# Kernel tuning notes

Hardware: AMD Instinct MI355X
Metric: run time of the kernel (lower is better)

## Reference

```python
import jax, jax.numpy as jnp
import numpy as np

B, S, D, H, DFF, L, R, V = 2, 1024, 1024, 16, 4096, 2, 3, 32000
HD = D // H


def layer_norm(x, g, b, eps=1e-5):
    mu = jnp.mean(x, axis=-1, keepdims=True)
    var = jnp.var(x, axis=-1, keepdims=True)
    return (x - mu) / jnp.sqrt(var + eps) * g + b


def recursion_block(x, mask, Wqkv, bqkv, Wo, bo, W1, b1, W2, b2, ln1_g, ln1_b, ln2_g, ln2_b):
    # shared pre-LN transformer stack of L layers, applied once per recursion step
    Bc, Sc, _ = x.shape
    scale = 1.0 / np.sqrt(HD).astype(np.float32)
    for l in range(L):
        h = layer_norm(x, ln1_g[l], ln1_b[l])
        qkv = h @ Wqkv[l] + bqkv[l]
        q, k, v = jnp.split(qkv, 3, axis=-1)
        q = q.reshape(Bc, Sc, H, HD).transpose(0, 2, 1, 3)
        k = k.reshape(Bc, Sc, H, HD).transpose(0, 2, 1, 3)
        v = v.reshape(Bc, Sc, H, HD).transpose(0, 2, 1, 3)
        scores = jnp.einsum('bhqd,bhkd->bhqk', q, k) * scale + mask
        attn = jax.nn.softmax(scores, axis=-1)
        o = jnp.einsum('bhqk,bhkd->bhqd', attn, v).transpose(0, 2, 1, 3).reshape(Bc, Sc, D)
        x = x + o @ Wo[l] + bo[l]
        h2 = layer_norm(x, ln2_g[l], ln2_b[l])
        x = x + jax.nn.gelu(h2 @ W1[l] + b1[l]) @ W2[l] + b2[l]
    return x


def setup_inputs() -> dict:
    key = jax.random.key(0)
    ks = jax.random.split(key, 12)
    n = lambda k, shape: (jax.random.normal(k, shape, jnp.float32) * 0.02)
    return {
        'input_ids': jax.random.randint(ks[0], (B, S), 0, V),
        'token_embed': n(ks[1], (V, D)),
        'pos_embed': n(ks[2], (S, D)),
        'Wqkv': n(ks[3], (L, D, 3 * D)), 'bqkv': jnp.zeros((L, 3 * D), jnp.float32),
        'Wo': n(ks[4], (L, D, D)), 'bo': jnp.zeros((L, D), jnp.float32),
        'W1': n(ks[5], (L, D, DFF)), 'b1': jnp.zeros((L, DFF), jnp.float32),
        'W2': n(ks[6], (L, DFF, D)), 'b2': jnp.zeros((L, D), jnp.float32),
        'ln1_g': jnp.ones((L, D), jnp.float32), 'ln1_b': jnp.zeros((L, D), jnp.float32),
        'ln2_g': jnp.ones((L, D), jnp.float32), 'ln2_b': jnp.zeros((L, D), jnp.float32),
        'final_g': jnp.ones((D,), jnp.float32), 'final_b': jnp.zeros((D,), jnp.float32),
        'Wr': n(ks[7], (D, R)), 'br': jnp.zeros((R,), jnp.float32),
    }


def reference(input_ids, token_embed, pos_embed, Wqkv, bqkv, Wo, bo, W1, b1, W2, b2,
              ln1_g, ln1_b, ln2_g, ln2_b, final_g, final_b, Wr, br):
    h = token_embed[input_ids] + pos_embed[None, :, :]            # [B,S,D]
    mask = jnp.where(jnp.tril(jnp.ones((S, S), bool)), 0.0, -jnp.inf)[None, None]  # [1,1,S,S]
    # token-choice router on detached hidden states
    rlogits = jax.lax.stop_gradient(h) @ Wr + br                  # [B,S,R]
    probs = jax.nn.softmax(rlogits, axis=-1)
    depth_map = jnp.argmax(rlogits, axis=-1) + 1                  # depths in 1..R
    importance = probs.mean(axis=(0, 1))
    router_loss = R * jnp.sum(importance ** 2)                    # load-balance aux loss
    res = h
    for step in range(R):
        step_mask = depth_map >= step + 1                         # [B,S] bool
        upd = recursion_block(res, mask, Wqkv, bqkv, Wo, bo, W1, b1, W2, b2,
                              ln1_g, ln1_b, ln2_g, ln2_b)
        res = jnp.where(step_mask[..., None], upd, res)
    hf = layer_norm(res, final_g, final_b)
    logits = hf @ token_embed.T                                   # tied lm_head
    return logits, depth_map, router_loss
```

## Files before the change

kernel.cpp:

```cpp
#include <hip/hip_runtime.h>
#include <hip/hip_bf16.h>

#define DD 1024
#define SS 1024
#define BB 2
#define HH 16
#define DFFN 4096
#define LLAYERS 2
#define RSTEPS 3
#define VV 32000
#define NTOK (BB*SS)

typedef __attribute__((ext_vector_type(8))) short s16x8;
typedef __attribute__((ext_vector_type(8))) __bf16 bf16x8;
typedef __attribute__((ext_vector_type(4))) float f32x4;

__device__ __forceinline__ unsigned short f2bf(float f) {
  unsigned int u = __float_as_uint(f);
  u += 0x7FFFu + ((u >> 16) & 1u);
  return (unsigned short)(u >> 16);
}

__device__ __forceinline__ f32x4 mfma16(s16x8 a, s16x8 b, f32x4 c) {
  return __builtin_amdgcn_mfma_f32_16x16x32_bf16(
      __builtin_bit_cast(bf16x8, a), __builtin_bit_cast(bf16x8, b), c, 0, 0, 0);
}

__device__ __forceinline__ void gload16(const unsigned short* g, unsigned short* l) {
  __builtin_amdgcn_global_load_lds(
      (const __attribute__((address_space(1))) unsigned int*)(const void*)g,
      (__attribute__((address_space(3))) unsigned int*)(void*)l, 16, 0, 0);
}

#define BAR()  asm volatile("s_barrier" ::: "memory")
#define LGK0() do { asm volatile("s_waitcnt lgkmcnt(0)" ::: "memory"); \
                    __builtin_amdgcn_sched_barrier(0); } while (0)
#define VM4()  asm volatile("s_waitcnt vmcnt(4)" ::: "memory")
#define VM0()  asm volatile("s_waitcnt vmcnt(0)" ::: "memory")

__global__ __launch_bounds__(256) void wtrans_all_kernel(
    const float* __restrict__ Wqkv, const float* __restrict__ Wo,
    const float* __restrict__ W1, const float* __restrict__ W2,
    unsigned short* __restrict__ WqkvT, unsigned short* __restrict__ WoT,
    unsigned short* __restrict__ W1T, unsigned short* __restrict__ W2T) {
  const int bid = blockIdx.x;
  const float* src; unsigned short* dst; int Kd, Nd, local;
  if (bid < 1536) {
    int l = bid >> 9 >= 1 ? (bid >= 768) : 0; l = (bid >= 768);
    local = bid - l * 768;
    src = Wqkv + (long)l * DD * 3 * DD; dst = WqkvT + (long)l * 3 * DD * DD;
    Kd = DD; Nd = 3 * DD;
  } else if (bid < 2048) {
    int l = (bid - 1536) >> 8; local = (bid - 1536) & 255;
    src = Wo + (long)l * DD * DD; dst = WoT + (long)l * DD * DD;
    Kd = DD; Nd = DD;
  } else if (bid < 4096) {
    int l = (bid - 2048) >> 10; local = (bid - 2048) & 1023;
    src = W1 + (long)l * DD * DFFN; dst = W1T + (long)l * DFFN * DD;
    Kd = DD; Nd = DFFN;
  } else {
    int l = (bid - 4096) >> 10; local = (bid - 4096) & 1023;
    src = W2 + (long)l * DFFN * DD; dst = W2T + (long)l * DD * DFFN;
    Kd = DFFN; Nd = DD;
  }
  const int tn = Nd >> 6;
  const int n0 = (local % tn) * 64, k0 = (local / tn) * 64;
  __shared__ unsigned short t[64][68];
  const int tid = threadIdx.x;
#pragma unroll
  for (int c = 0; c < 4; ++c) {
    int p = tid + c * 256;
    int kr = p >> 4, nc = (p & 15) * 4;
    float4 v = *(const float4*)(src + (long)(k0 + kr) * Nd + n0 + nc);
    t[nc + 0][kr] = f2bf(v.x);
    t[nc + 1][kr] = f2bf(v.y);
    t[nc + 2][kr] = f2bf(v.z);
    t[nc + 3][kr] = f2bf(v.w);
  }
  __syncthreads();
#pragma unroll
  for (int c = 0; c < 4; ++c) {
    int p = tid + c * 256;
    int nr = p >> 4, kc = (p & 15) * 4;
    ushort4 o;
    o.x = t[nr][kc]; o.y = t[nr][kc + 1]; o.z = t[nr][kc + 2]; o.w = t[nr][kc + 3];
    *(ushort4*)(dst + (long)(n0 + nr) * Kd + k0 + kc) = o;
  }
}

__global__ __launch_bounds__(256) void bconv_kernel(
    const float* __restrict__ src, unsigned short* __restrict__ dst) {
  long i = ((long)blockIdx.x * 256 + threadIdx.x) * 8;
  float4 v0 = *(const float4*)(src + i);
  float4 v1 = *(const float4*)(src + i + 4);
  ushort4 a, b;
  a.x = f2bf(v0.x); a.y = f2bf(v0.y); a.z = f2bf(v0.z); a.w = f2bf(v0.w);
  b.x = f2bf(v1.x); b.y = f2bf(v1.y); b.z = f2bf(v1.z); b.w = f2bf(v1.w);
  *(ushort4*)(dst + i) = a;
  *(ushort4*)(dst + i + 4) = b;
}

__global__ __launch_bounds__(256) void embed_router_kernel(
    const int* __restrict__ ids, const float* __restrict__ te,
    const float* __restrict__ pe, const float* __restrict__ Wr,
    const float* __restrict__ br, float* __restrict__ res,
    float* __restrict__ probs, float* __restrict__ depth_ws,
    float* __restrict__ out_depth) {
  int row = blockIdx.x;
  int s = row & (SS - 1);
  int id = ids[row];
  int t = threadIdx.x;
  int d = t * 4;
  float4 a = *(const float4*)(te + (long)id * DD + d);
  float4 p = *(const float4*)(pe + (long)s * DD + d);
  float4 o; o.x = a.x + p.x; o.y = a.y + p.y; o.z = a.z + p.z; o.w = a.w + p.w;
  *(float4*)(res + (long)row * DD + d) = o;
  float a0 = 0.f, a1 = 0.f, a2 = 0.f;
  float hv[4] = {o.x, o.y, o.z, o.w};
#pragma unroll
  for (int j = 0; j < 4; ++j) {
    int dd = d + j;
    a0 += hv[j] * Wr[dd * 3 + 0];
    a1 += hv[j] * Wr[dd * 3 + 1];
    a2 += hv[j] * Wr[dd * 3 + 2];
  }
  for (int off = 32; off; off >>= 1) {
    a0 += __shfl_down(a0, off);
    a1 += __shfl_down(a1, off);
    a2 += __shfl_down(a2, off);
  }
  __shared__ float red[4][3];
  int wave = t >> 6;
  if ((t & 63) == 0) { red[wave][0] = a0; red[wave][1] = a1; red[wave][2] = a2; }
  __syncthreads();
  if (t == 0) {
    a0 = red[0][0] + red[1][0] + red[2][0] + red[3][0] + br[0];
    a1 = red[0][1] + red[1][1] + red[2][1] + red[3][1] + br[1];
    a2 = red[0][2] + red[1][2] + red[2][2] + red[3][2] + br[2];
    float m = fmaxf(a0, fmaxf(a1, a2));
    float e0 = expf(a0 - m), e1 = expf(a1 - m), e2 = expf(a2 - m);
    float inv = 1.f / (e0 + e1 + e2);
    probs[row * 3 + 0] = e0 * inv;
    probs[row * 3 + 1] = e1 * inv;
    probs[row * 3 + 2] = e2 * inv;
    int am = 0; float bv = a0;
    if (a1 > bv) { bv = a1; am = 1; }
    if (a2 > bv) { bv = a2; am = 2; }
    float dm = (float)(am + 1);
    depth_ws[row] = dm;
    out_depth[row] = dm;
  }
}

__global__ __launch_bounds__(256) void router_finalize_kernel(
    const float* __restrict__ probs, float* __restrict__ out_loss) {
  __shared__ float red[256][3];
  int t = threadIdx.x;
  float s0 = 0.f, s1 = 0.f, s2 = 0.f;
  for (int r = t; r < NTOK; r += 256) {
    s0 += probs[r * 3 + 0]; s1 += probs[r * 3 + 1]; s2 += probs[r * 3 + 2];
  }
  red[t][0] = s0; red[t][1] = s1; red[t][2] = s2;
  __syncthreads();
  for (int off = 128; off; off >>= 1) {
    if (t < off) {
      red[t][0] += red[t + off][0];
      red[t][1] += red[t + off][1];
      red[t][2] += red[t + off][2];
    }
    __syncthreads();
  }
  if (t == 0) {
    float i0 = red[0][0] / NTOK, i1 = red[0][1] / NTOK, i2 = red[0][2] / NTOK;
    out_loss[0] = (float)RSTEPS * (i0 * i0 + i1 * i1 + i2 * i2);
  }
}

__global__ __launch_bounds__(256) void ln_kernel(
    const float* __restrict__ x, const float* __restrict__ g,
    const float* __restrict__ b, unsigned short* __restrict__ y) {
  int row = blockIdx.x;
  int t = threadIdx.x;
  float4 v = *(const float4*)(x + (long)row * DD + t * 4);
  float s = v.x + v.y + v.z + v.w;
  float q = v.x * v.x + v.y * v.y + v.z * v.z + v.w * v.w;
  for (int off = 32; off; off >>= 1) {
    s += __shfl_down(s, off);
    q += __shfl_down(q, off);
  }
  __shared__ float rs[4], rq[4];
  int wave = t >> 6;
  if ((t & 63) == 0) { rs[wave] = s; rq[wave] = q; }
  __syncthreads();
  float S_ = rs[0] + rs[1] + rs[2] + rs[3];
  float Q_ = rq[0] + rq[1] + rq[2] + rq[3];
  float mu = S_ * (1.f / DD);
  float var = Q_ * (1.f / DD) - mu * mu;
  float rstd = rsqrtf(var + 1e-5f);
  int d = t * 4;
  float4 gg = *(const float4*)(g + d);
  float4 bb = *(const float4*)(b + d);
  ushort4 ov;
  ov.x = f2bf((v.x - mu) * rstd * gg.x + bb.x);
  ov.y = f2bf((v.y - mu) * rstd * gg.y + bb.y);
  ov.z = f2bf((v.z - mu) * rstd * gg.z + bb.z);
  ov.w = f2bf((v.w - mu) * rstd * gg.w + bb.w);
  *(ushort4*)(y + (long)row * DD + d) = ov;
}

__device__ __forceinline__ void stageA8(unsigned short* S, int buf, int qm,
    const unsigned short* A, int lda, long m0, int kt, int tid) {
  unsigned short* dst = S + buf * 32768 + qm * 8192;
#pragma unroll
  for (int c = 0; c < 2; ++c) {
    int idx = tid + c * 512;
    int L = (idx << 4) ^ (((idx >> 5) & 1) << 5);
    int band = L >> 13, row = (L >> 7) & 63, kel = (L & 127) >> 1;
    gload16(A + (m0 + band * 128 + qm * 64 + row) * (long)lda + kt * 64 + kel,
            dst + idx * 8);
  }
}

__device__ __forceinline__ void stageB8(unsigned short* S, int buf, int qn,
    const unsigned short* Bt, int ldb, long n0, int kt, int tid) {
  unsigned short* dst = S + buf * 32768 + 16384 + qn * 8192;
#pragma unroll
  for (int c = 0; c < 2; ++c) {
    int idx = tid + c * 512;
    int L = (idx << 4) ^ (((idx >> 5) & 1) << 5);
    int band = L >> 12, row = (L >> 7) & 31, kel = (L & 127) >> 1;
    gload16(Bt + (n0 + band * 64 + qn * 32 + row) * (long)ldb + kt * 64 + kel,
            dst + idx * 8);
  }
}

__device__ __forceinline__ void read_af8(const unsigned short* S, int base,
    int wm, int l16, int g, s16x8 af[2][4]) {
  const int swz = ((l16 >> 2) & 1) << 5;
#pragma unroll
  for (int kk = 0; kk < 2; ++kk)
#pragma unroll
    for (int mf = 0; mf < 4; ++mf) {
      int L = (wm * 8192 + (mf * 16 + l16) * 128 + (kk * 32 + g * 8) * 2) ^ swz;
      af[kk][mf] = *(const s16x8*)(S + base + (L >> 1));
    }
}

__device__ __forceinline__ void read_bf8(const unsigned short* S, int base,
    int wn, int l16, int g, s16x8 bf[2][2]) {
  const int swz = ((l16 >> 2) & 1) << 5;
#pragma unroll
  for (int kk = 0; kk < 2; ++kk)
#pragma unroll
    for (int nf = 0; nf < 2; ++nf) {
      int L = (wn * 4096 + (nf * 16 + l16) * 128 + (kk * 32 + g * 8) * 2) ^ swz;
      bf[kk][nf] = *(const s16x8*)(S + base + (L >> 1));
    }
}

template<int QM, int QN>
__device__ __forceinline__ void do_mfma8(f32x4 acc[8][4],
    const s16x8 af[2][4], const s16x8 bf[2][2]) {
  __builtin_amdgcn_s_setprio(1);
#pragma unroll
  for (int kk = 0; kk < 2; ++kk)
#pragma unroll
    for (int mf = 0; mf < 4; ++mf)
#pragma unroll
      for (int nf = 0; nf < 2; ++nf)
        acc[QM * 4 + mf][QN * 2 + nf] =
            mfma16(af[kk][mf], bf[kk][nf], acc[QM * 4 + mf][QN * 2 + nf]);
  __builtin_amdgcn_s_setprio(0);
}

template<int CBF16, int BIAS, int GELU_ACT>
__global__ __launch_bounds__(512, 1) void gemm256_kernel(
    const unsigned short* __restrict__ A, int lda,
    const unsigned short* __restrict__ Bt, int ldb,
    void* __restrict__ Cv, int ldc,
    const float* __restrict__ bias, int K, int Mblocks) {
  __shared__ unsigned short S[65536];
  const int tid = threadIdx.x;
  const int lane = tid & 63, wave = tid >> 6;
  const int g = lane >> 4, l16 = lane & 15;
  const int wm = wave >> 2, wn = wave & 3;
  const int nwg = gridDim.x * gridDim.y;
  const int orig = blockIdx.x + blockIdx.y * gridDim.x;
  const int q = nwg >> 3, r = nwg & 7;
  const int xcd = orig & 7, loc = orig >> 3;
  const int wgid = (xcd < r ? xcd * (q + 1) : r * (q + 1) + (xcd - r) * q) + loc;
  const long m0 = (long)(wgid % Mblocks) * 256;
  const long n0 = (long)(wgid / Mblocks) * 256;

  f32x4 acc[8][4] = {};
  s16x8 af[2][4], bf[2][2];
  const int NI = K >> 7;

  stageA8(S, 0, 0, A, lda, m0, 0, tid);
  stageA8(S, 0, 1, A, lda, m0, 0, tid);
  stageB8(S, 0, 0, Bt, ldb, n0, 0, tid);
  stageB8(S, 0, 1, Bt, ldb, n0, 0, tid);
  stageA8(S, 1, 0, A, lda, m0, 1, tid);
  stageB8(S, 1, 1, Bt, ldb, n0, 1, tid);
  VM4(); BAR();

  for (int i = 0; i < NI; ++i) {
    const int kt1 = 2 * i + 1, kt2 = 2 * i + 2, kt3 = 2 * i + 3;
    const bool more = (i + 1 < NI);
    read_af8(S, 0, wm, l16, g, af);
    read_bf8(S, 16384, wn, l16, g, bf);
    stageA8(S, 1, 1, A, lda, m0, kt1, tid);
    BAR(); LGK0();
    do_mfma8<0, 0>(acc, af, bf);
    BAR();
    read_bf8(S, 16384 + 8192, wn, l16, g, bf);
    stageB8(S, 1, 0, Bt, ldb, n0, kt1, tid);
    BAR(); LGK0();
    do_mfma8<0, 1>(acc, af, bf);
    BAR();
    read_af8(S, 8192, wm, l16, g, af);
    if (more) stageA8(S, 0, 0, A, lda, m0, kt2, tid);
    BAR(); LGK0();
    do_mfma8<1, 1>(acc, af, bf);
    BAR();
    read_bf8(S, 16384, wn, l16, g, bf);
    if (more) stageB8(S, 0, 1, Bt, ldb, n0, kt2, tid);
    BAR(); LGK0();
    do_mfma8<1, 0>(acc, af, bf);
    if (more) { VM4(); } else { VM0(); }
    BAR();
    read_af8(S, 32768, wm, l16, g, af);
    read_bf8(S, 32768 + 16384, wn, l16, g, bf);
    if (more) stageA8(S, 0, 1, A, lda, m0, kt2, tid);
    BAR(); LGK0();
    do_mfma8<0, 0>(acc, af, bf);
    BAR();
    read_bf8(S, 32768 + 16384 + 8192, wn, l16, g, bf);
    if (more) stageB8(S, 0, 0, Bt, ldb, n0, kt2, tid);
    BAR(); LGK0();
    do_mfma8<0, 1>(acc, af, bf);
    BAR();
    read_af8(S, 32768 + 8192, wm, l16, g, af);
    if (more) stageA8(S, 1, 0, A, lda, m0, kt3, tid);
    BAR(); LGK0();
    do_mfma8<1, 1>(acc, af, bf);
    BAR();
    read_bf8(S, 32768 + 16384, wn, l16, g, bf);
    if (more) stageB8(S, 1, 1, Bt, ldb, n0, kt3, tid);
    BAR(); LGK0();
    do_mfma8<1, 0>(acc, af, bf);
    VM4(); BAR();
  }

#pragma unroll
  for (int mf = 0; mf < 8; ++mf) {
#pragma unroll
    for (int nf = 0; nf < 4; ++nf) {
      long row0 = m0 + wm * 128 + mf * 16 + g * 4;
      long col = n0 + wn * 64 + nf * 16 + l16;
      float bv = BIAS ? bias[col] : 0.f;
#pragma unroll
      for (int rr = 0; rr < 4; ++rr) {
        float v = acc[mf][nf][rr] + bv;
        if (GELU_ACT) {
          float x3 = v * v * v;
          v = 0.5f * v * (1.f + tanhf(0.7978845608028654f * (v + 0.044715f * x3)));
        }
        if (CBF16) ((unsigned short*)Cv)[(row0 + rr) * (long)ldc + col] = f2bf(v);
        else       ((float*)Cv)[(row0 + rr) * (long)ldc + col] = v;
      }
    }
  }
}

template<int BN, int CBF16, int BIAS, int RESID, int GELU_ACT, int SELW>
__global__ __launch_bounds__(256) void gemm128_kernel(
    const unsigned short* __restrict__ A, int lda,
    const unsigned short* __restrict__ Bt, int ldb,
    void* __restrict__ Cv, int ldc,
    const float* __restrict__ bias,
    const float* __restrict__ resid, int ldr,
    const float* __restrict__ depth_ws, float stepf,
    int K) {
  constexpr int BM = 128;
  constexpr int WN = BN / 2;
  constexpr int MR = 4;
  constexpr int NR = WN / 16;
  __shared__ unsigned short As[BM * 64];
  __shared__ unsigned short Bs[BN * 64];
  const int tid = threadIdx.x;
  const int lane = tid & 63, wave = tid >> 6;
  const int g = lane >> 4, l16 = lane & 15;
  const int wr = wave >> 1, wc = wave & 1;
  int lin = blockIdx.x + blockIdx.y * gridDim.x;
  int per = (gridDim.x * gridDim.y) >> 3;
  int v = (lin & 7) * per + (lin >> 3);
  const long m0 = (long)(v % gridDim.y) * BM;
  const long n0 = (long)(v / gridDim.y) * BN;
  f32x4 acc[MR][NR] = {};
  for (int k0 = 0; k0 < K; k0 += 64) {
    __syncthreads();
#pragma unroll
    for (int c = 0; c < BM / 32; ++c) {
      int p = tid + c * 256;
      int r = p >> 3, kq = (p & 7) * 8;
      gload16(A + (m0 + r) * (long)lda + k0 + kq, &As[p * 8]);
    }
#pragma unroll
    for (int c = 0; c < BN / 32; ++c) {
      int p = tid + c * 256;
      int r = p >> 3, kq = (p & 7) * 8;
      gload16(Bt + (n0 + r) * (long)ldb + k0 + kq, &Bs[p * 8]);
    }
    __syncthreads();
#pragma unroll
    for (int kk = 0; kk < 2; ++kk) {
      s16x8 af[MR], bf[NR];
#pragma unroll
      for (int m = 0; m < MR; ++m)
        af[m] = *(const s16x8*)&As[(wr * 64 + m * 16 + l16) * 64 + kk * 32 + g * 8];
#pragma unroll
      for (int n = 0; n < NR; ++n)
        bf[n] = *(const s16x8*)&Bs[(wc * WN + n * 16 + l16) * 64 + kk * 32 + g * 8];
#pragma unroll
      for (int m = 0; m < MR; ++m)
#pragma unroll
        for (int n = 0; n < NR; ++n)
          acc[m][n] = mfma16(af[m], bf[n], acc[m][n]);
    }
  }
#pragma unroll
  for (int m = 0; m < MR; ++m) {
#pragma unroll
    for (int n = 0; n < NR; ++n) {
      long row_base = m0 + wr * 64 + m * 16 + g * 4;
      long col = n0 + wc * WN + n * 16 + l16;
      float bv = BIAS ? bias[col] : 0.f;
#pragma unroll
      for (int r = 0; r < 4; ++r) {
        long row = row_base + r;
        float vv = acc[m][n][r] + bv;
        if (RESID) vv += resid[row * (long)ldr + col];
        if (GELU_ACT) {
          float x3 = vv * vv * vv;
          vv = 0.5f * vv * (1.f + tanhf(0.7978845608028654f * (vv + 0.044715f * x3)));
        }
        if (SELW) {
          if (depth_ws[row] >= stepf)
            ((float*)Cv)[row * (long)ldc + col] = vv;
        } else if (CBF16) {
          ((unsigned short*)Cv)[row * (long)ldc + col] = f2bf(vv);
        } else {
          ((float*)Cv)[row * (long)ldc + col] = vv;
        }
      }
    }
  }
}

__global__ __launch_bounds__(256) void vtrans_kernel(
    const unsigned short* __restrict__ qkv, unsigned short* __restrict__ vt) {
  __shared__ unsigned short t[64][72];
  const int s0 = blockIdx.x * 64;
  const int bh = blockIdx.y;
  const int b = bh >> 4, h = bh & 15;
  const int tid = threadIdx.x;
  const long rowbase = (long)b * SS;
#pragma unroll
  for (int c = 0; c < 2; ++c) {
    int p = tid + c * 256;
    int sr = p >> 3, d8 = (p & 7) * 8;
    s16x8 v = *(const s16x8*)(qkv + (rowbase + s0 + sr) * 3072 + 2048 + h * 64 + d8);
#pragma unroll
    for (int j = 0; j < 8; ++j) t[d8 + j][sr] = v[j];
  }
  __syncthreads();
#pragma unroll
  for (int c = 0; c < 2; ++c) {
    int p = tid + c * 256;
    int d = p >> 3, s8 = (p & 7) * 8;
    *(s16x8*)(vt + ((long)bh * 64 + d) * SS + s0 + s8) = *(const s16x8*)&t[d][s8];
  }
}

__global__ __launch_bounds__(256) void attn_kernel(
    const unsigned short* __restrict__ qkv,
    const unsigned short* __restrict__ vt,
    unsigned short* __restrict__ o) {
  __shared__ unsigned short Ks[2][64 * 64];
  __shared__ unsigned short Vs[2][64 * 64];
  __shared__ unsigned short Pl[4][16][72];
  const int qb = blockIdx.x;
  const int bh = blockIdx.y;
  const int b = bh >> 4, h = bh & 15;
  const int tid = threadIdx.x, wave = tid >> 6, lane = tid & 63;
  const int g = lane >> 4, l16 = lane & 15;
  const float NEG_INF = -__builtin_inff();
  const int q0 = qb * 64;
  const int qrw = q0 + wave * 16;
  const long rowbase = (long)b * SS;
  const unsigned short* kbase = qkv + rowbase * 3072 + 1024 + h * 64;
  const unsigned short* vbase = vt + (long)bh * 64 * SS;

  const unsigned short* qptr = qkv + (rowbase + qrw + l16) * 3072 + h * 64;
  s16x8 qf0 = *(const s16x8*)(qptr + g * 8);
  s16x8 qf1 = *(const s16x8*)(qptr + 32 + g * 8);

  f32x4 oacc[4] = {};
  float mrun = NEG_INF, lrun = 0.f;

  const int ntile = q0 / 64 + 1;

#pragma unroll
  for (int c = 0; c < 2; ++c) {
    int idx = tid + c * 256;
    int r = idx >> 3;
    int bo = (idx & 7) * 16;
    int sw = (bo ^ ((r & 7) << 4)) >> 1;
    gload16(kbase + (long)r * 3072 + sw, &Ks[0][idx * 8]);
    gload16(vbase + (long)r * SS + 0 + sw, &Vs[0][idx * 8]);
  }
  asm volatile("s_waitcnt vmcnt(0)" ::: "memory");
  __syncthreads();

  for (int t = 0; t < ntile; ++t) {
    const int cur = t & 1;
    const int kv0 = t * 64;
    const unsigned short* ks_cur = &Ks[cur][0];
    const unsigned short* vs_cur = &Vs[cur][0];
    if (t + 1 < ntile) {
      const int kvn = kv0 + 64;
#pragma unroll
      for (int c = 0; c < 2; ++c) {
        int idx = tid + c * 256;
        int r = idx >> 3;
        int bo = (idx & 7) * 16;
        int sw = (bo ^ ((r & 7) << 4)) >> 1;
        gload16(kbase + (long)(kvn + r) * 3072 + sw, &Ks[cur ^ 1][idx * 8]);
        gload16(vbase + (long)r * SS + kvn + sw, &Vs[cur ^ 1][idx * 8]);
      }
    }
    f32x4 accs[4] = {};
#pragma unroll
    for (int ks = 0; ks < 2; ++ks) {
#pragma unroll
      for (int kvb = 0; kvb < 4; ++kvb) {
        int row = kvb * 16 + l16;
        int bo = ((ks * 64 + g * 16) ^ ((l16 & 7) << 4)) >> 1;
        s16x8 kf = *(const s16x8*)&ks_cur[row * 64 + bo];
        accs[kvb] = mfma16(kf, ks ? qf1 : qf0, accs[kvb]);
      }
    }
    const bool needmask = (kv0 + 63 > qrw);
    const int qabs = qrw + l16;
    float sv[4][4];
    float mloc = NEG_INF;
#pragma unroll
    for (int kvb = 0; kvb < 4; ++kvb) {
#pragma unroll
      for (int r = 0; r < 4; ++r) {
        float vv = accs[kvb][r] * 0.125f;
        if (needmask) {
          int kva = kv0 + kvb * 16 + g * 4 + r;
          if (kva > qabs) vv = NEG_INF;
        }
        sv[kvb][r] = vv;
        mloc = fmaxf(mloc, vv);
      }
    }
    mloc = fmaxf(mloc, __shfl_xor(mloc, 16));
    mloc = fmaxf(mloc, __shfl_xor(mloc, 32));
    float mnew = fmaxf(mrun, mloc);
    float alpha = __expf(mrun - mnew);
    float lsum = 0.f;
#pragma unroll
    for (int kvb = 0; kvb < 4; ++kvb) {
      float p0 = __expf(sv[kvb][0] - mnew);
      float p1 = __expf(sv[kvb][1] - mnew);
      float p2 = __expf(sv[kvb][2] - mnew);
      float p3 = __expf(sv[kvb][3] - mnew);
      lsum += (p0 + p1) + (p2 + p3);
      unsigned int w0 = (unsigned)f2bf(p0) | ((unsigned)f2bf(p1) << 16);
      unsigned int w1 = (unsigned)f2bf(p2) | ((unsigned)f2bf(p3) << 16);
      uint2 pw; pw.x = w0; pw.y = w1;
      *(uint2*)&Pl[wave][l16][kvb * 16 + g * 4] = pw;
    }
    lsum += __shfl_xor(lsum, 16);
    lsum += __shfl_xor(lsum, 32);
    lrun = lrun * alpha + lsum;
    mrun = mnew;
    float mult[4];
#pragma unroll
    for (int r = 0; r < 4; ++r) mult[r] = __shfl(alpha, g * 4 + r);
#pragma unroll
    for (int nd = 0; nd < 4; ++nd)
#pragma unroll
      for (int r = 0; r < 4; ++r) oacc[nd][r] *= mult[r];
#pragma unroll
    for (int kh = 0; kh < 2; ++kh) {
      s16x8 pa = *(const s16x8*)&Pl[wave][l16][kh * 32 + g * 8];
#pragma unroll
      for (int nd = 0; nd < 4; ++nd) {
        int row = nd * 16 + l16;
        int bo = ((kh * 64 + g * 16) ^ ((l16 & 7) << 4)) >> 1;
        s16x8 vf = *(const s16x8*)&vs_cur[row * 64 + bo];
        oacc[nd] = mfma16(pa, vf, oacc[nd]);
      }
    }
    asm volatile("s_waitcnt vmcnt(0)" ::: "memory");
    __syncthreads();
  }
  unsigned short* ob = o + (rowbase + qrw) * 1024 + h * 64;
#pragma unroll
  for (int r = 0; r < 4; ++r) {
    float lr = __shfl(lrun, g * 4 + r);
    float inv = 1.f / lr;
#pragma unroll
    for (int nd = 0; nd < 4; ++nd)
      ob[(long)(g * 4 + r) * 1024 + nd * 16 + l16] = f2bf(oacc[nd][r] * inv);
  }
}

extern "C" void kernel_launch(void* const* d_in, const int* in_sizes, int n_in,
                              void* d_out, int out_size, void* d_ws, size_t ws_size,
                              hipStream_t stream) {
  (void)in_sizes; (void)n_in; (void)out_size; (void)ws_size;
  const int*   ids  = (const int*)d_in[0];
  const float* te   = (const float*)d_in[1];
  const float* pe   = (const float*)d_in[2];
  const float* Wqkv = (const float*)d_in[3];
  const float* bqkv = (const float*)d_in[4];
  const float* Wo   = (const float*)d_in[5];
  const float* bo   = (const float*)d_in[6];
  const float* W1   = (const float*)d_in[7];
  const float* b1   = (const float*)d_in[8];
  const float* W2   = (const float*)d_in[9];
  const float* b2   = (const float*)d_in[10];
  const float* ln1g = (const float*)d_in[11];
  const float* ln1b = (const float*)d_in[12];
  const float* ln2g = (const float*)d_in[13];
  const float* ln2b = (const float*)d_in[14];
  const float* fing = (const float*)d_in[15];
  const float* finb = (const float*)d_in[16];
  const float* Wr   = (const float*)d_in[17];
  const float* br   = (const float*)d_in[18];

  float* logits    = (float*)d_out;
  float* out_depth = logits + (long)NTOK * VV;
  float* out_loss  = out_depth + NTOK;

  char* w = (char*)d_ws;
  float* res            = (float*)w;          w += (long)NTOK * DD * 4;
  float* x              = (float*)w;          w += (long)NTOK * DD * 4;
  unsigned short* hbuf  = (unsigned short*)w; w += (long)NTOK * DD * 2;
  unsigned short* qkvb  = (unsigned short*)w; w += (long)NTOK * 3 * DD * 2;
  unsigned short* obuf  = (unsigned short*)w; w += (long)NTOK * DD * 2;
  unsigned short* ffn1  = (unsigned short*)w; w += (long)NTOK * DFFN * 2;
  unsigned short* vtb   = (unsigned short*)w; w += (long)BB * HH * 64 * SS * 2;
  float* probs          = (float*)w;          w += (long)NTOK * 3 * 4;
  float* depth_ws       = (float*)w;          w += (long)NTOK * 4;
  unsigned short* WqkvT = (unsigned short*)w; w += (long)LLAYERS * 3 * DD * DD * 2;
  unsigned short* WoT   = (unsigned short*)w; w += (long)LLAYERS * DD * DD * 2;
  unsigned short* W1T   = (unsigned short*)w; w += (long)LLAYERS * DFFN * DD * 2;
  unsigned short* W2T   = (unsigned short*)w; w += (long)LLAYERS * DD * DFFN * 2;
  unsigned short* teb   = (unsigned short*)w; w += (long)VV * DD * 2;

  wtrans_all_kernel<<<6144, 256, 0, stream>>>(Wqkv, Wo, W1, W2,
                                              WqkvT, WoT, W1T, W2T);
  bconv_kernel<<<(long)VV * DD / 2048, 256, 0, stream>>>(te, teb);

  embed_router_kernel<<<NTOK, 256, 0, stream>>>(ids, te, pe, Wr, br,
                                                res, probs, depth_ws, out_depth);
  router_finalize_kernel<<<1, 256, 0, stream>>>(probs, out_loss);

  for (int step = 0; step < RSTEPS; ++step) {
    for (int l = 0; l < LLAYERS; ++l) {
      const float* xin = (l == 0) ? res : x;
      ln_kernel<<<NTOK, 256, 0, stream>>>(xin, ln1g + l * DD, ln1b + l * DD, hbuf);
      gemm128_kernel<128, 1, 1, 0, 0, 0><<<dim3(3 * DD / 128, NTOK / 128), 256, 0, stream>>>(
          hbuf, DD, WqkvT + (long)l * 3 * DD * DD, DD, qkvb, 3 * DD,
          bqkv + (long)l * 3 * DD, nullptr, 0, nullptr, 0.f, DD);
      vtrans_kernel<<<dim3(SS / 64, BB * HH), 256, 0, stream>>>(qkvb, vtb);
      attn_kernel<<<dim3(SS / 64, BB * HH), 256, 0, stream>>>(qkvb, vtb, obuf);
      gemm128_kernel<64, 0, 1, 1, 0, 0><<<dim3(DD / 64, NTOK / 128), 256, 0, stream>>>(
          obuf, DD, WoT + (long)l * DD * DD, DD, x, DD,
          bo + (long)l * DD, xin, DD, nullptr, 0.f, DD);
      ln_kernel<<<NTOK, 256, 0, stream>>>(x, ln2g + l * DD, ln2b + l * DD, hbuf);
      gemm128_kernel<128, 1, 1, 0, 1, 0><<<dim3(DFFN / 128, NTOK / 128), 256, 0, stream>>>(
          hbuf, DD, W1T + (long)l * DFFN * DD, DD, ffn1, DFFN,
          b1 + (long)l * DFFN, nullptr, 0, nullptr, 0.f, DD);
      if (l == 0) {
        gemm128_kernel<64, 0, 1, 1, 0, 0><<<dim3(DD / 64, NTOK / 128), 256, 0, stream>>>(
            ffn1, DFFN, W2T + (long)l * DD * DFFN, DFFN, x, DD,
            b2 + (long)l * DD, x, DD, nullptr, 0.f, DFFN);
      } else {
        gemm128_kernel<64, 0, 1, 1, 0, 1><<<dim3(DD / 64, NTOK / 128), 256, 0, stream>>>(
            ffn1, DFFN, W2T + (long)l * DD * DFFN, DFFN, res, DD,
            b2 + (long)l * DD, x, DD, depth_ws, (float)(step + 1), DFFN);
      }
    }
  }
  ln_kernel<<<NTOK, 256, 0, stream>>>(res, fing, finb, hbuf);
  gemm256_kernel<0, 0, 0><<<dim3(VV / 256, NTOK / 256), 512, 0, stream>>>(
      hbuf, DD, teb, DD, logits, VV, nullptr, DD, NTOK / 256);
}
```

Measured before the change: 1.460 ms.

## Fuse V transpose into QKV GEMM epilogue, widen attention blocks, merge conversion kernels

The QKV GEMM epilogue now writes the V columns straight into the transposed per-head layout, which removes the separate vtrans kernel and one round trip of V through memory. The attention kernel goes to 512 threads covering 128 query rows per block, so each K/V tile loaded into shared memory is reused by eight waves instead of four. The embedding bf16 conversion is folded into the weight-transpose launch as extra blocks, saving one launch. The V scatter uses 8-byte strided stores that may coalesce worse, and the larger attention blocks halve the grid and process an extra diagonal tile per block.

```diff
diff --git a/kernel.cpp b/kernel.cpp
--- a/kernel.cpp
+++ b/kernel.cpp
@@ -41,12 +41,26 @@
 __global__ __launch_bounds__(256) void wtrans_all_kernel(
     const float* __restrict__ Wqkv, const float* __restrict__ Wo,
     const float* __restrict__ W1, const float* __restrict__ W2,
+    const float* __restrict__ te,
     unsigned short* __restrict__ WqkvT, unsigned short* __restrict__ WoT,
-    unsigned short* __restrict__ W1T, unsigned short* __restrict__ W2T) {
+    unsigned short* __restrict__ W1T, unsigned short* __restrict__ W2T,
+    unsigned short* __restrict__ teb) {
   const int bid = blockIdx.x;
+  const int tid = threadIdx.x;
+  if (bid >= 6144) {
+    long i = ((long)(bid - 6144) * 256 + tid) * 8;
+    float4 v0 = *(const float4*)(te + i);
+    float4 v1 = *(const float4*)(te + i + 4);
+    ushort4 a, b;
+    a.x = f2bf(v0.x); a.y = f2bf(v0.y); a.z = f2bf(v0.z); a.w = f2bf(v0.w);
+    b.x = f2bf(v1.x); b.y = f2bf(v1.y); b.z = f2bf(v1.z); b.w = f2bf(v1.w);
+    *(ushort4*)(teb + i) = a;
+    *(ushort4*)(teb + i + 4) = b;
+    return;
+  }
   const float* src; unsigned short* dst; int Kd, Nd, local;
   if (bid < 1536) {
-    int l = bid >> 9 >= 1 ? (bid >= 768) : 0; l = (bid >= 768);
+    int l = (bid >= 768);
     local = bid - l * 768;
     src = Wqkv + (long)l * DD * 3 * DD; dst = WqkvT + (long)l * 3 * DD * DD;
     Kd = DD; Nd = 3 * DD;
@@ -66,7 +80,6 @@
   const int tn = Nd >> 6;
   const int n0 = (local % tn) * 64, k0 = (local / tn) * 64;
   __shared__ unsigned short t[64][68];
-  const int tid = threadIdx.x;
 #pragma unroll
   for (int c = 0; c < 4; ++c) {
     int p = tid + c * 256;
@@ -86,18 +99,6 @@
     o.x = t[nr][kc]; o.y = t[nr][kc + 1]; o.z = t[nr][kc + 2]; o.w = t[nr][kc + 3];
     *(ushort4*)(dst + (long)(n0 + nr) * Kd + k0 + kc) = o;
   }
-}
-
-__global__ __launch_bounds__(256) void bconv_kernel(
-    const float* __restrict__ src, unsigned short* __restrict__ dst) {
-  long i = ((long)blockIdx.x * 256 + threadIdx.x) * 8;
-  float4 v0 = *(const float4*)(src + i);
-  float4 v1 = *(const float4*)(src + i + 4);
-  ushort4 a, b;
-  a.x = f2bf(v0.x); a.y = f2bf(v0.y); a.z = f2bf(v0.z); a.w = f2bf(v0.w);
-  b.x = f2bf(v1.x); b.y = f2bf(v1.y); b.z = f2bf(v1.z); b.w = f2bf(v1.w);
-  *(ushort4*)(dst + i) = a;
-  *(ushort4*)(dst + i + 4) = b;
 }
 
 __global__ __launch_bounds__(256) void embed_router_kernel(
@@ -373,7 +374,7 @@
   }
 }
 
-template<int BN, int CBF16, int BIAS, int RESID, int GELU_ACT, int SELW>
+template<int BN, int CBF16, int BIAS, int RESID, int GELU_ACT, int SELW, int QKVW>
 __global__ __launch_bounds__(256) void gemm128_kernel(
     const unsigned short* __restrict__ A, int lda,
     const unsigned short* __restrict__ Bt, int ldb,
@@ -381,6 +382,7 @@
     const float* __restrict__ bias,
     const float* __restrict__ resid, int ldr,
     const float* __restrict__ depth_ws, float stepf,
+    unsigned short* __restrict__ vtw,
     int K) {
   constexpr int BM = 128;
   constexpr int WN = BN / 2;
@@ -429,6 +431,7 @@
           acc[m][n] = mfma16(af[m], bf[n], acc[m][n]);
     }
   }
+  const bool vblk = QKVW && (n0 >= 2048);
 #pragma unroll
   for (int m = 0; m < MR; ++m) {
 #pragma unroll
@@ -436,6 +439,7 @@
       long row_base = m0 + wr * 64 + m * 16 + g * 4;
       long col = n0 + wc * WN + n * 16 + l16;
       float bv = BIAS ? bias[col] : 0.f;
+      float vv4[4];
 #pragma unroll
       for (int r = 0; r < 4; ++r) {
         long row = row_base + r;
@@ -445,58 +449,49 @@
           float x3 = vv * vv * vv;
           vv = 0.5f * vv * (1.f + tanhf(0.7978845608028654f * (vv + 0.044715f * x3)));
         }
-        if (SELW) {
-          if (depth_ws[row] >= stepf)
-            ((float*)Cv)[row * (long)ldc + col] = vv;
-        } else if (CBF16) {
-          ((unsigned short*)Cv)[row * (long)ldc + col] = f2bf(vv);
-        } else {
-          ((float*)Cv)[row * (long)ldc + col] = vv;
+        vv4[r] = vv;
+      }
+      if (QKVW && vblk) {
+        int rel = (int)col - 2048;
+        int h = rel >> 6, d = rel & 63;
+        int b = (int)(row_base >> 10);
+        int s = (int)(row_base & 1023);
+        ushort4 o;
+        o.x = f2bf(vv4[0]); o.y = f2bf(vv4[1]);
+        o.z = f2bf(vv4[2]); o.w = f2bf(vv4[3]);
+        *(ushort4*)(vtw + (((long)(b * 16 + h) * 64 + d) * SS + s)) = o;
+      } else {
+#pragma unroll
+        for (int r = 0; r < 4; ++r) {
+          long row = row_base + r;
+          if (SELW) {
+            if (depth_ws[row] >= stepf)
+              ((float*)Cv)[row * (long)ldc + col] = vv4[r];
+          } else if (CBF16) {
+            ((unsigned short*)Cv)[row * (long)ldc + col] = f2bf(vv4[r]);
+          } else {
+            ((float*)Cv)[row * (long)ldc + col] = vv4[r];
+          }
         }
       }
     }
   }
 }
 
-__global__ __launch_bounds__(256) void vtrans_kernel(
-    const unsigned short* __restrict__ qkv, unsigned short* __restrict__ vt) {
-  __shared__ unsigned short t[64][72];
-  const int s0 = blockIdx.x * 64;
-  const int bh = blockIdx.y;
-  const int b = bh >> 4, h = bh & 15;
-  const int tid = threadIdx.x;
-  const long rowbase = (long)b * SS;
-#pragma unroll
-  for (int c = 0; c < 2; ++c) {
-    int p = tid + c * 256;
-    int sr = p >> 3, d8 = (p & 7) * 8;
-    s16x8 v = *(const s16x8*)(qkv + (rowbase + s0 + sr) * 3072 + 2048 + h * 64 + d8);
-#pragma unroll
-    for (int j = 0; j < 8; ++j) t[d8 + j][sr] = v[j];
-  }
-  __syncthreads();
-#pragma unroll
-  for (int c = 0; c < 2; ++c) {
-    int p = tid + c * 256;
-    int d = p >> 3, s8 = (p & 7) * 8;
-    *(s16x8*)(vt + ((long)bh * 64 + d) * SS + s0 + s8) = *(const s16x8*)&t[d][s8];
-  }
-}
-
-__global__ __launch_bounds__(256) void attn_kernel(
+__global__ __launch_bounds__(512) void attn_kernel(
     const unsigned short* __restrict__ qkv,
     const unsigned short* __restrict__ vt,
     unsigned short* __restrict__ o) {
   __shared__ unsigned short Ks[2][64 * 64];
   __shared__ unsigned short Vs[2][64 * 64];
-  __shared__ unsigned short Pl[4][16][72];
+  __shared__ unsigned short Pl[8][16][72];
   const int qb = blockIdx.x;
   const int bh = blockIdx.y;
   const int b = bh >> 4, h = bh & 15;
   const int tid = threadIdx.x, wave = tid >> 6, lane = tid & 63;
   const int g = lane >> 4, l16 = lane & 15;
   const float NEG_INF = -__builtin_inff();
-  const int q0 = qb * 64;
+  const int q0 = qb * 128;
   const int qrw = q0 + wave * 16;
   const long rowbase = (long)b * SS;
   const unsigned short* kbase = qkv + rowbase * 3072 + 1024 + h * 64;
@@ -509,16 +504,14 @@
   f32x4 oacc[4] = {};
   float mrun = NEG_INF, lrun = 0.f;
 
-  const int ntile = q0 / 64 + 1;
-
-#pragma unroll
-  for (int c = 0; c < 2; ++c) {
-    int idx = tid + c * 256;
-    int r = idx >> 3;
-    int bo = (idx & 7) * 16;
+  const int ntile = q0 / 64 + 2;
+
+  {
+    int r = tid >> 3;
+    int bo = (tid & 7) * 16;
     int sw = (bo ^ ((r & 7) << 4)) >> 1;
-    gload16(kbase + (long)r * 3072 + sw, &Ks[0][idx * 8]);
-    gload16(vbase + (long)r * SS + 0 + sw, &Vs[0][idx * 8]);
+    gload16(kbase + (long)r * 3072 + sw, &Ks[0][tid * 8]);
+    gload16(vbase + (long)r * SS + 0 + sw, &Vs[0][tid * 8]);
   }
   asm volatile("s_waitcnt vmcnt(0)" ::: "memory");
   __syncthreads();
@@ -530,15 +523,11 @@
     const unsigned short* vs_cur = &Vs[cur][0];
     if (t + 1 < ntile) {
       const int kvn = kv0 + 64;
-#pragma unroll
-      for (int c = 0; c < 2; ++c) {
-        int idx = tid + c * 256;
-        int r = idx >> 3;
-        int bo = (idx & 7) * 16;
-        int sw = (bo ^ ((r & 7) << 4)) >> 1;
-        gload16(kbase + (long)(kvn + r) * 3072 + sw, &Ks[cur ^ 1][idx * 8]);
-        gload16(vbase + (long)r * SS + kvn + sw, &Vs[cur ^ 1][idx * 8]);
-      }
+      int r = tid >> 3;
+      int bo = (tid & 7) * 16;
+      int sw = (bo ^ ((r & 7) << 4)) >> 1;
+      gload16(kbase + (long)(kvn + r) * 3072 + sw, &Ks[cur ^ 1][tid * 8]);
+      gload16(vbase + (long)r * SS + kvn + sw, &Vs[cur ^ 1][tid * 8]);
     }
     f32x4 accs[4] = {};
 #pragma unroll
@@ -665,9 +654,8 @@
   unsigned short* W2T   = (unsigned short*)w; w += (long)LLAYERS * DD * DFFN * 2;
   unsigned short* teb   = (unsigned short*)w; w += (long)VV * DD * 2;
 
-  wtrans_all_kernel<<<6144, 256, 0, stream>>>(Wqkv, Wo, W1, W2,
-                                              WqkvT, WoT, W1T, W2T);
-  bconv_kernel<<<(long)VV * DD / 2048, 256, 0, stream>>>(te, teb);
+  wtrans_all_kernel<<<6144 + 16000, 256, 0, stream>>>(
+      Wqkv, Wo, W1, W2, te, WqkvT, WoT, W1T, W2T, teb);
 
   embed_router_kernel<<<NTOK, 256, 0, stream>>>(ids, te, pe, Wr, br,
                                                 res, probs, depth_ws, out_depth);
@@ -677,26 +665,25 @@
     for (int l = 0; l < LLAYERS; ++l) {
       const float* xin = (l == 0) ? res : x;
       ln_kernel<<<NTOK, 256, 0, stream>>>(xin, ln1g + l * DD, ln1b + l * DD, hbuf);
-      gemm128_kernel<128, 1, 1, 0, 0, 0><<<dim3(3 * DD / 128, NTOK / 128), 256, 0, stream>>>(
+      gemm128_kernel<128, 1, 1, 0, 0, 0, 1><<<dim3(3 * DD / 128, NTOK / 128), 256, 0, stream>>>(
           hbuf, DD, WqkvT + (long)l * 3 * DD * DD, DD, qkvb, 3 * DD,
-          bqkv + (long)l * 3 * DD, nullptr, 0, nullptr, 0.f, DD);
-      vtrans_kernel<<<dim3(SS / 64, BB * HH), 256, 0, stream>>>(qkvb, vtb);
-      attn_kernel<<<dim3(SS / 64, BB * HH), 256, 0, stream>>>(qkvb, vtb, obuf);
-      gemm128_kernel<64, 0, 1, 1, 0, 0><<<dim3(DD / 64, NTOK / 128), 256, 0, stream>>>(
+          bqkv + (long)l * 3 * DD, nullptr, 0, nullptr, 0.f, vtb, DD);
+      attn_kernel<<<dim3(SS / 128, BB * HH), 512, 0, stream>>>(qkvb, vtb, obuf);
+      gemm128_kernel<64, 0, 1, 1, 0, 0, 0><<<dim3(DD / 64, NTOK / 128), 256, 0, stream>>>(
           obuf, DD, WoT + (long)l * DD * DD, DD, x, DD,
-          bo + (long)l * DD, xin, DD, nullptr, 0.f, DD);
+          bo + (long)l * DD, xin, DD, nullptr, 0.f, nullptr, DD);
       ln_kernel<<<NTOK, 256, 0, stream>>>(x, ln2g + l * DD, ln2b + l * DD, hbuf);
-      gemm128_kernel<128, 1, 1, 0, 1, 0><<<dim3(DFFN / 128, NTOK / 128), 256, 0, stream>>>(
+      gemm128_kernel<128, 1, 1, 0, 1, 0, 0><<<dim3(DFFN / 128, NTOK / 128), 256, 0, stream>>>(
           hbuf, DD, W1T + (long)l * DFFN * DD, DD, ffn1, DFFN,
-          b1 + (long)l * DFFN, nullptr, 0, nullptr, 0.f, DD);
+          b1 + (long)l * DFFN, nullptr, 0, nullptr, 0.f, nullptr, DD);
       if (l == 0) {
-        gemm128_kernel<64, 0, 1, 1, 0, 0><<<dim3(DD / 64, NTOK / 128), 256, 0, stream>>>(
+        gemm128_kernel<64, 0, 1, 1, 0, 0, 0><<<dim3(DD / 64, NTOK / 128), 256, 0, stream>>>(
             ffn1, DFFN, W2T + (long)l * DD * DFFN, DFFN, x, DD,
-            b2 + (long)l * DD, x, DD, nullptr, 0.f, DFFN);
+            b2 + (long)l * DD, x, DD, nullptr, 0.f, nullptr, DFFN);
       } else {
-        gemm128_kernel<64, 0, 1, 1, 0, 1><<<dim3(DD / 64, NTOK / 128), 256, 0, stream>>>(
+        gemm128_kernel<64, 0, 1, 1, 0, 1, 0><<<dim3(DD / 64, NTOK / 128), 256, 0, stream>>>(
             ffn1, DFFN, W2T + (long)l * DD * DFFN, DFFN, res, DD,
-            b2 + (long)l * DD, x, DD, depth_ws, (float)(step + 1), DFFN);
+            b2 + (long)l * DD, x, DD, depth_ws, (float)(step + 1), nullptr, DFFN);
       }
     }
   }
```

New measurement: 1.437 ms (median of 2 runs). About the same (-1.5%).
